# Kernel tuning notes

Measured on AMD Instinct MI355X. Metric: run time of the kernel, lower is better.

Reference implementation:

```python
import jax, jax.numpy as jnp
import numpy as np

B, L, D = 4, 2048, 2048
NH, HD, K = 32, 64, 16
LR = 1.0
EPS = 1e-6


def ln_fwd(x, gamma, beta):
    mu = x.mean(-1, keepdims=True)
    var = jnp.var(x, axis=-1, keepdims=True)
    x_hat = (x - mu) / jnp.sqrt(var + EPS)
    return gamma * x_hat + beta


def ln_fused_l2_bwd(x, target, gamma, beta):
    # grad of 0.5*||LN(x)-target||^2 wrt x (matches LayerNormFunction.backward
    # with grad_output = LN(x) - target)
    d = x.shape[-1]
    mu = x.mean(-1, keepdims=True)
    var = jnp.var(x, axis=-1, keepdims=True)
    std = jnp.sqrt(var + EPS)
    x_hat = (x - mu) / std
    y = gamma * x_hat + beta
    g = (y - target) * gamma
    return (d * g - g.sum(-1, keepdims=True) - x_hat * (g * x_hat).sum(-1, keepdims=True)) / (d * std)


def setup_inputs() -> dict:
    key = jax.random.key(0)
    ks = jax.random.split(key, 12)
    s = 0.02
    return {
        "hidden_states": jax.random.normal(ks[0], (B, L, D), jnp.float32),
        "Wq": jax.random.normal(ks[1], (D, D), jnp.float32) * s,
        "Wk": jax.random.normal(ks[2], (D, D), jnp.float32) * s,
        "Wv": jax.random.normal(ks[3], (D, D), jnp.float32) * s,
        "Wo": jax.random.normal(ks[4], (D, D), jnp.float32) * s,
        "linear_weight": jax.random.normal(ks[5], (NH, 1, D), jnp.float32) * s,
        "linear_bias": jnp.zeros((NH, 1), jnp.float32),
        "ln_weight": jnp.ones((NH, HD), jnp.float32),
        "ln_bias": jnp.zeros((NH, HD), jnp.float32),
        "W1_init": jax.random.normal(ks[6], (NH, HD, HD), jnp.float32) * s,
        "b1_init": jnp.zeros((NH, 1, HD), jnp.float32),
    }


def reference(hidden_states, Wq, Wk, Wv, Wo, linear_weight, linear_bias,
              ln_weight, ln_bias, W1_init, b1_init):
    Bq, Lq, Dq = hidden_states.shape
    n_chunk = Lq // K

    def split(x):  # [B,L,D] -> [B,NH,n_chunk,K,HD]
        return x.reshape(Bq, n_chunk, K, NH, HD).transpose(0, 3, 1, 2, 4)

    XC = split(hidden_states @ Wq.T)
    XB = split(hidden_states @ Wk.T)
    XA = split(hidden_states @ Wv.T)

    # inner-loop learning-rate coefficient: [B,NH,n_chunk,K,1]
    X = hidden_states.reshape(Bq, n_chunk, K, Dq)
    ilr = jnp.einsum('bnkd,hd->bhnk', X, linear_weight[:, 0, :]) + linear_bias[:, 0][None, :, None, None]
    ilr_gated = jax.nn.sigmoid(ilr)[..., None]
    token_idx = 1.0 / jnp.arange(1, K + 1, dtype=hidden_states.dtype)
    coeff = (LR * token_idx).reshape(1, 1, 1, K, 1) * ilr_gated / HD

    ln_w = ln_weight.reshape(1, NH, 1, HD)
    ln_b = ln_bias.reshape(1, NH, 1, HD)
    mask = jnp.tril(jnp.ones((K, K), hidden_states.dtype))

    W1 = jnp.broadcast_to(W1_init[None], (Bq, NH, HD, HD))
    b1 = jnp.broadcast_to(b1_init[None], (Bq, NH, 1, HD))

    def step(carry, inp):
        W1, b1 = carry
        xc, xb, xa, co = inp  # [B,NH,K,HD], co: [B,NH,K,1]
        Z1 = xb @ W1 + b1
        grad = ln_fused_l2_bwd(Z1, xa - xb, ln_w, ln_b)  # [B,NH,K,HD]
        Attn = mask * jnp.einsum('bhkf,bhjf->bhkj', xc, xb)
        E = mask * co.transpose(0, 1, 3, 2)  # E[i,j] = coeff_j * (j<=i)
        b1_bar = b1 - E @ grad
        Z1_bar = xc @ W1 - (Attn * E) @ grad + b1_bar
        W1_new = W1 - jnp.einsum('bhkf,bhkg->bhfg', co * xb, grad)
        b1_new = b1 - (co * grad).sum(-2, keepdims=True)
        out = xc + ln_fwd(Z1_bar, ln_w, ln_b)
        return (W1_new, b1_new), out

    xs = (XC.transpose(2, 0, 1, 3, 4), XB.transpose(2, 0, 1, 3, 4),
          XA.transpose(2, 0, 1, 3, 4), coeff.transpose(2, 0, 1, 3, 4))
    (_, _), outs = jax.lax.scan(step, (W1, b1), xs)
    # outs: [n_chunk,B,NH,K,HD] -> [B,L,D]
    XCW = outs.transpose(1, 0, 3, 2, 4).reshape(Bq, Lq, Dq)
    return XCW @ Wo.T
```

## Files before the change

kernel.cpp:

```cpp
#include <hip/hip_runtime.h>


typedef __attribute__((ext_vector_type(4))) float float4v;
typedef __attribute__((ext_vector_type(8))) __bf16 bf16x8;
typedef __attribute__((ext_vector_type(4))) short short4v;
typedef __attribute__((ext_vector_type(4))) unsigned int uint4v;

__device__ __forceinline__ unsigned short f2bf(float f) {
  unsigned int u = __builtin_bit_cast(unsigned int, f);
  u += 0x7FFFu + ((u >> 16) & 1u);
  return (unsigned short)(u >> 16);
}
__device__ __forceinline__ float bf2f(unsigned short s) {
  unsigned int u = ((unsigned int)s) << 16;
  return __builtin_bit_cast(float, u);
}
__device__ __forceinline__ void lds_load16(const void* g, void* l) {
  __builtin_amdgcn_global_load_lds((const __attribute__((address_space(1))) void*)g,
                                   (__attribute__((address_space(3))) void*)l, 16, 0, 0);
}

__device__ __forceinline__ void store_out(float* p, float v) { *p = v; }
__device__ __forceinline__ void store_out(unsigned short* p, float v) { *p = f2bf(v); }

template <typename OUT>
__global__ __launch_bounds__(256) void gemm_bt(
    const unsigned short* __restrict__ A, const unsigned short* __restrict__ B,
    OUT* __restrict__ C, int M, int N, int K) {
  __shared__ unsigned short sA[128 * 32];
  __shared__ unsigned short sB[128 * 32];
  const int tid = threadIdx.x;
  const int wave = tid >> 6;
  const int lane = tid & 63;
  const int quad = lane >> 4;
  const int l15 = lane & 15;
  const int wm = (wave >> 1) * 64;
  const int wn = (wave & 1) * 64;
  const int bm = blockIdx.y * 128;
  const int bn = blockIdx.x * 128;

  float4v acc[4][4];
#pragma unroll
  for (int i = 0; i < 4; ++i)
#pragma unroll
    for (int j = 0; j < 4; ++j) acc[i][j] = (float4v){0.f, 0.f, 0.f, 0.f};

  const int srow = tid >> 2;
  const int scol = (tid & 3) * 8;
  const unsigned short* aptr = A + (size_t)(bm + srow) * K + scol;
  const unsigned short* bptr = B + (size_t)(bn + srow) * K + scol;
  unsigned short* sAw0 = &sA[wave * 512];
  unsigned short* sAw1 = &sA[2048 + wave * 512];
  unsigned short* sBw0 = &sB[wave * 512];
  unsigned short* sBw1 = &sB[2048 + wave * 512];
  const size_t astep = (size_t)64 * K;

  for (int kt = 0; kt < K; kt += 32) {
    __syncthreads();
    lds_load16(aptr + kt, sAw0);
    lds_load16(aptr + kt + astep, sAw1);
    lds_load16(bptr + kt, sBw0);
    lds_load16(bptr + kt + astep, sBw1);
    __syncthreads();
    bf16x8 af[4], bf[4];
#pragma unroll
    for (int i = 0; i < 4; ++i)
      af[i] = *(const bf16x8*)&sA[(wm + i * 16 + l15) * 32 + quad * 8];
#pragma unroll
    for (int j = 0; j < 4; ++j)
      bf[j] = *(const bf16x8*)&sB[(wn + j * 16 + l15) * 32 + quad * 8];
#pragma unroll
    for (int i = 0; i < 4; ++i)
#pragma unroll
      for (int j = 0; j < 4; ++j)
        acc[i][j] = __builtin_amdgcn_mfma_f32_16x16x32_bf16(af[i], bf[j], acc[i][j], 0, 0, 0);
  }

#pragma unroll
  for (int i = 0; i < 4; ++i) {
    const int row0 = bm + wm + i * 16 + quad * 4;
#pragma unroll
    for (int j = 0; j < 4; ++j) {
      const int col = bn + wn + j * 16 + l15;
#pragma unroll
      for (int r = 0; r < 4; ++r)
        store_out(&C[(size_t)(row0 + r) * N + col], acc[i][j][r]);
    }
  }
}

__global__ __launch_bounds__(256) void f32_to_bf16_k(const float* __restrict__ s,
                                                     unsigned short* __restrict__ d, int n) {
  const int i = (blockIdx.x * 256 + threadIdx.x) * 8;
  if (i >= n) return;
  const float4v a = *(const float4v*)(s + i);
  const float4v b = *(const float4v*)(s + i + 4);
  uint4v o;
  o[0] = (unsigned int)f2bf(a[0]) | ((unsigned int)f2bf(a[1]) << 16);
  o[1] = (unsigned int)f2bf(a[2]) | ((unsigned int)f2bf(a[3]) << 16);
  o[2] = (unsigned int)f2bf(b[0]) | ((unsigned int)f2bf(b[1]) << 16);
  o[3] = (unsigned int)f2bf(b[2]) | ((unsigned int)f2bf(b[3]) << 16);
  *(uint4v*)(d + i) = o;
}

__global__ __launch_bounds__(256) void coeff_k(const unsigned short* __restrict__ ilr,
                                               const float* __restrict__ lb,
                                               float* __restrict__ coeff) {
  const int gid = blockIdx.x * 256 + threadIdx.x;
  const int row = gid >> 5;
  const int h = gid & 31;
  const float v = bf2f(ilr[row * 128 + h]) + lb[h];
  const float sig = 1.0f / (1.0f + __expf(-v));
  const int b = row >> 11;
  const int pos = row & 2047;
  const int cc = pos >> 4;
  const int k = pos & 15;
  coeff[((((size_t)b * 32 + h) * 128 + cc) << 4) + k] = sig / (64.0f * (float)(k + 1));
}

__global__ __launch_bounds__(64, 1) void ttt_scan(
    const unsigned short* __restrict__ XC, const unsigned short* __restrict__ XB,
    const unsigned short* __restrict__ XA, const float* __restrict__ coeff,
    const float* __restrict__ lnw, const float* __restrict__ lnb,
    const float* __restrict__ W1i, const float* __restrict__ b1i,
    unsigned short* __restrict__ XCW) {
  const int b = blockIdx.x >> 5;
  const int h = blockIdx.x & 31;
  const int lane = threadIdx.x;
  const int quad = lane >> 4;
  const int l15 = lane & 15;

  __shared__ float sW1T[64 * 68];
  __shared__ float sXCs[16 * 68];
  __shared__ float sXBs[16 * 68];
  __shared__ float sTs[16 * 68];
  __shared__ float sAttn[16 * 20];
  __shared__ float sB1[64];

  float gam[4], bet[4];
#pragma unroll
  for (int nt = 0; nt < 4; ++nt) {
    gam[nt] = lnw[h * 64 + nt * 16 + l15];
    bet[nt] = lnb[h * 64 + nt * 16 + l15];
  }
  float4v W1r[16];
#pragma unroll
  for (int mt = 0; mt < 4; ++mt)
#pragma unroll
    for (int nt = 0; nt < 4; ++nt) {
      float4v v;
#pragma unroll
      for (int r = 0; r < 4; ++r)
        v[r] = W1i[(size_t)h * 4096 + (size_t)(mt * 16 + quad * 4 + r) * 64 + nt * 16 + l15];
      W1r[mt * 4 + nt] = v;
    }
  sB1[lane] = b1i[h * 64 + lane];

  const int srow = lane >> 2;
  const int scol = (lane & 3) * 16;
  const size_t hdoff = (size_t)h * 64;
  const size_t browoff = (size_t)b * 2048;
  const size_t cobase = (((size_t)b * 32 + h) * 128) * 16;
  const float inv64 = 1.0f / 64.0f;
  const float4v zero4 = {0.f, 0.f, 0.f, 0.f};

  uint4v pxc0, pxc1, pxb0, pxb1, pxa0, pxa1;
  float pco;
  {
    const size_t goff = (browoff + (size_t)srow) * 2048 + hdoff + scol;
    pxc0 = *(const uint4v*)(XC + goff);
    pxc1 = *(const uint4v*)(XC + goff + 8);
    pxb0 = *(const uint4v*)(XB + goff);
    pxb1 = *(const uint4v*)(XB + goff + 8);
    pxa0 = *(const uint4v*)(XA + goff);
    pxa1 = *(const uint4v*)(XA + goff + 8);
    pco = coeff[cobase + l15];
  }

  for (int c = 0; c < 128; ++c) {
    const uint4v xc0 = pxc0, xc1 = pxc1, xb0 = pxb0, xb1 = pxb1, xa0 = pxa0, xa1 = pxa1;
    const float co = pco;
    {
      const int cn = (c < 127) ? c + 1 : 127;
      const size_t goff = (browoff + (size_t)(cn * 16 + srow)) * 2048 + hdoff + scol;
      pxc0 = *(const uint4v*)(XC + goff);
      pxc1 = *(const uint4v*)(XC + goff + 8);
      pxb0 = *(const uint4v*)(XB + goff);
      pxb1 = *(const uint4v*)(XB + goff + 8);
      pxa0 = *(const uint4v*)(XA + goff);
      pxa1 = *(const uint4v*)(XA + goff + 8);
      pco = coeff[cobase + (size_t)cn * 16 + l15];
    }

    float xcv[16], xbv[16], xav[16];
#pragma unroll
    for (int t2 = 0; t2 < 4; ++t2) {
      xcv[t2 * 2] = __builtin_bit_cast(float, xc0[t2] << 16);
      xcv[t2 * 2 + 1] = __builtin_bit_cast(float, xc0[t2] & 0xFFFF0000u);
      xcv[8 + t2 * 2] = __builtin_bit_cast(float, xc1[t2] << 16);
      xcv[8 + t2 * 2 + 1] = __builtin_bit_cast(float, xc1[t2] & 0xFFFF0000u);
      xbv[t2 * 2] = __builtin_bit_cast(float, xb0[t2] << 16);
      xbv[t2 * 2 + 1] = __builtin_bit_cast(float, xb0[t2] & 0xFFFF0000u);
      xbv[8 + t2 * 2] = __builtin_bit_cast(float, xb1[t2] << 16);
      xbv[8 + t2 * 2 + 1] = __builtin_bit_cast(float, xb1[t2] & 0xFFFF0000u);
      xav[t2 * 2] = __builtin_bit_cast(float, xa0[t2] << 16);
      xav[t2 * 2 + 1] = __builtin_bit_cast(float, xa0[t2] & 0xFFFF0000u);
      xav[8 + t2 * 2] = __builtin_bit_cast(float, xa1[t2] << 16);
      xav[8 + t2 * 2 + 1] = __builtin_bit_cast(float, xa1[t2] & 0xFFFF0000u);
    }
    const int sb = srow * 68 + scol;
#pragma unroll
    for (int e = 0; e < 16; ++e) {
      sXCs[sb + e] = xcv[e];
      sXBs[sb + e] = xbv[e];
      sTs[sb + e] = xav[e] - xbv[e];
    }
#pragma unroll
    for (int mt = 0; mt < 4; ++mt)
#pragma unroll
      for (int nt = 0; nt < 4; ++nt)
        *(float4v*)&sW1T[(nt * 16 + l15) * 68 + mt * 16 + quad * 4] = W1r[mt * 4 + nt];

    bf16x8 xbf[2], xcf[2];
#pragma unroll
    for (int hh = 0; hh < 2; ++hh) {
      const float4v pb0 = *(const float4v*)&sXBs[l15 * 68 + hh * 32 + quad * 8];
      const float4v pb1 = *(const float4v*)&sXBs[l15 * 68 + hh * 32 + quad * 8 + 4];
      const float4v pc0 = *(const float4v*)&sXCs[l15 * 68 + hh * 32 + quad * 8];
      const float4v pc1 = *(const float4v*)&sXCs[l15 * 68 + hh * 32 + quad * 8 + 4];
      bf16x8 fb, fc;
#pragma unroll
      for (int r = 0; r < 4; ++r) {
        fb[r] = (__bf16)pb0[r]; fb[4 + r] = (__bf16)pb1[r];
        fc[r] = (__bf16)pc0[r]; fc[4 + r] = (__bf16)pc1[r];
      }
      xbf[hh] = fb; xcf[hh] = fc;
    }
    bf16x8 w1f[4][2];
#pragma unroll
    for (int nt = 0; nt < 4; ++nt)
#pragma unroll
      for (int hh = 0; hh < 2; ++hh) {
        const float4v p0 = *(const float4v*)&sW1T[(nt * 16 + l15) * 68 + hh * 32 + quad * 8];
        const float4v p1 = *(const float4v*)&sW1T[(nt * 16 + l15) * 68 + hh * 32 + quad * 8 + 4];
        bf16x8 f;
#pragma unroll
        for (int r = 0; r < 4; ++r) { f[r] = (__bf16)p0[r]; f[4 + r] = (__bf16)p1[r]; }
        w1f[nt][hh] = f;
      }
    float cof[4];
#pragma unroll
    for (int r = 0; r < 4; ++r) cof[r] = __shfl(co, quad * 4 + r);
    float b1v[4];
#pragma unroll
    for (int nt = 0; nt < 4; ++nt) b1v[nt] = sB1[nt * 16 + l15];

    float4v z[4];
#pragma unroll
    for (int nt = 0; nt < 4; ++nt) {
      float4v t = __builtin_amdgcn_mfma_f32_16x16x32_bf16(xbf[0], w1f[nt][0], zero4, 0, 0, 0);
      t = __builtin_amdgcn_mfma_f32_16x16x32_bf16(xbf[1], w1f[nt][1], t, 0, 0, 0);
#pragma unroll
      for (int r = 0; r < 4; ++r) t[r] += b1v[nt];
      z[nt] = t;
    }

    float s1[4], s2[4];
#pragma unroll
    for (int r = 0; r < 4; ++r) {
      s1[r] = z[0][r] + z[1][r] + z[2][r] + z[3][r];
      s2[r] = z[0][r] * z[0][r] + z[1][r] * z[1][r] + z[2][r] * z[2][r] + z[3][r] * z[3][r];
    }
#pragma unroll
    for (int m = 1; m <= 8; m <<= 1)
#pragma unroll
      for (int r = 0; r < 4; ++r) {
        s1[r] += __shfl_xor(s1[r], m);
        s2[r] += __shfl_xor(s2[r], m);
      }
    float mu[4], rstd[4];
#pragma unroll
    for (int r = 0; r < 4; ++r) {
      mu[r] = s1[r] * inv64;
      const float var = s2[r] * inv64 - mu[r] * mu[r];
      rstd[r] = rsqrtf(var + 1e-6f);
    }
    float xh[4][4], gg[4][4];
#pragma unroll
    for (int nt = 0; nt < 4; ++nt)
#pragma unroll
      for (int r = 0; r < 4; ++r) {
        const float xhat = (z[nt][r] - mu[r]) * rstd[r];
        xh[nt][r] = xhat;
        const float y = gam[nt] * xhat + bet[nt];
        const float tgt = sTs[(quad * 4 + r) * 68 + nt * 16 + l15];
        gg[nt][r] = (y - tgt) * gam[nt];
      }
    float sg[4], sgx[4];
#pragma unroll
    for (int r = 0; r < 4; ++r) {
      sg[r] = gg[0][r] + gg[1][r] + gg[2][r] + gg[3][r];
      sgx[r] = gg[0][r] * xh[0][r] + gg[1][r] * xh[1][r] + gg[2][r] * xh[2][r] + gg[3][r] * xh[3][r];
    }
#pragma unroll
    for (int m = 1; m <= 8; m <<= 1)
#pragma unroll
      for (int r = 0; r < 4; ++r) {
        sg[r] += __shfl_xor(sg[r], m);
        sgx[r] += __shfl_xor(sgx[r], m);
      }
    float grad[4][4];
    short4v gradb[4];
#pragma unroll
    for (int nt = 0; nt < 4; ++nt)
#pragma unroll
      for (int r = 0; r < 4; ++r) {
        grad[nt][r] = (64.0f * gg[nt][r] - sg[r] - xh[nt][r] * sgx[r]) * (rstd[r] * inv64);
        gradb[nt][r] = (short)f2bf(grad[nt][r]);
      }

    float4v at = __builtin_amdgcn_mfma_f32_16x16x32_bf16(xcf[0], xbf[0], zero4, 0, 0, 0);
    at = __builtin_amdgcn_mfma_f32_16x16x32_bf16(xcf[1], xbf[1], at, 0, 0, 0);
#pragma unroll
    for (int r = 0; r < 4; ++r) sAttn[(quad * 4 + r) * 20 + l15] = at[r];
    const float4v av = *(const float4v*)&sAttn[l15 * 20 + quad * 4];
    short4v m1f;
#pragma unroll
    for (int jj = 0; jj < 4; ++jj) {
      const int k = quad * 4 + jj;
      const float e = (k <= l15) ? cof[jj] : 0.0f;
      m1f[jj] = (short)f2bf(-(av[jj] + 1.0f) * e);
    }

#pragma unroll
    for (int nt = 0; nt < 4; ++nt) {
      float4v t = __builtin_amdgcn_mfma_f32_16x16x32_bf16(xcf[0], w1f[nt][0], zero4, 0, 0, 0);
      t = __builtin_amdgcn_mfma_f32_16x16x32_bf16(xcf[1], w1f[nt][1], t, 0, 0, 0);
      t = __builtin_amdgcn_mfma_f32_16x16x16bf16_1k(m1f, gradb[nt], t, 0, 0, 0);
#pragma unroll
      for (int r = 0; r < 4; ++r) t[r] += b1v[nt];
      z[nt] = t;
    }

#pragma unroll
    for (int r = 0; r < 4; ++r) {
      s1[r] = z[0][r] + z[1][r] + z[2][r] + z[3][r];
      s2[r] = z[0][r] * z[0][r] + z[1][r] * z[1][r] + z[2][r] * z[2][r] + z[3][r] * z[3][r];
    }
#pragma unroll
    for (int m = 1; m <= 8; m <<= 1)
#pragma unroll
      for (int r = 0; r < 4; ++r) {
        s1[r] += __shfl_xor(s1[r], m);
        s2[r] += __shfl_xor(s2[r], m);
      }
#pragma unroll
    for (int r = 0; r < 4; ++r) {
      mu[r] = s1[r] * inv64;
      const float var = s2[r] * inv64 - mu[r] * mu[r];
      rstd[r] = rsqrtf(var + 1e-6f);
    }
#pragma unroll
    for (int nt = 0; nt < 4; ++nt)
#pragma unroll
      for (int r = 0; r < 4; ++r) {
        const float xhat = (z[nt][r] - mu[r]) * rstd[r];
        const float y = gam[nt] * xhat + bet[nt];
        const float o = sXCs[(quad * 4 + r) * 68 + nt * 16 + l15] + y;
        XCW[(browoff + (size_t)(c * 16 + quad * 4 + r)) * 2048 + hdoff + nt * 16 + l15] = f2bf(o);
      }

    float pb[4];
#pragma unroll
    for (int nt = 0; nt < 4; ++nt) {
      pb[nt] = cof[0] * grad[nt][0] + cof[1] * grad[nt][1] + cof[2] * grad[nt][2] + cof[3] * grad[nt][3];
      pb[nt] += __shfl_xor(pb[nt], 16);
      pb[nt] += __shfl_xor(pb[nt], 32);
    }
    if (lane < 16) {
#pragma unroll
      for (int nt = 0; nt < 4; ++nt) sB1[nt * 16 + lane] -= pb[nt];
    }

#pragma unroll
    for (int mt = 0; mt < 4; ++mt) {
      short4v caf;
#pragma unroll
      for (int jj = 0; jj < 4; ++jj)
        caf[jj] = (short)f2bf(-cof[jj] * sXBs[(quad * 4 + jj) * 68 + mt * 16 + l15]);
#pragma unroll
      for (int nt = 0; nt < 4; ++nt)
        W1r[mt * 4 + nt] =
            __builtin_amdgcn_mfma_f32_16x16x16bf16_1k(caf, gradb[nt], W1r[mt * 4 + nt], 0, 0, 0);
    }
  }
}

extern "C" void kernel_launch(void* const* d_in, const int* in_sizes, int n_in,
                              void* d_out, int out_size, void* d_ws, size_t ws_size,
                              hipStream_t stream) {
  const float* hs = (const float*)d_in[0];
  const float* Wq = (const float*)d_in[1];
  const float* Wk = (const float*)d_in[2];
  const float* Wv = (const float*)d_in[3];
  const float* Wo = (const float*)d_in[4];
  const float* lw = (const float*)d_in[5];
  const float* lb = (const float*)d_in[6];
  const float* lnw = (const float*)d_in[7];
  const float* lnb = (const float*)d_in[8];
  const float* W1i = (const float*)d_in[9];
  const float* b1i = (const float*)d_in[10];
  float* out = (float*)d_out;
  char* ws = (char*)d_ws;

  unsigned short* hsb = (unsigned short*)(ws);
  unsigned short* wqb = (unsigned short*)(ws + 33554432);
  unsigned short* wkb = (unsigned short*)(ws + 41943040);
  unsigned short* wvb = (unsigned short*)(ws + 50331648);
  unsigned short* wob = (unsigned short*)(ws + 58720256);
  unsigned short* lwb = (unsigned short*)(ws + 67108864);
  unsigned short* XCb = (unsigned short*)(ws + 67633152);
  unsigned short* XBb = (unsigned short*)(ws + 101187584);
  unsigned short* XAb = (unsigned short*)(ws + 134742016);
  unsigned short* ilrb = (unsigned short*)(ws + 168296448);
  float* coeff = (float*)(ws + 170393600);

  f32_to_bf16_k<<<8192, 256, 0, stream>>>(hs, hsb, 16777216);
  f32_to_bf16_k<<<2048, 256, 0, stream>>>(Wq, wqb, 4194304);
  f32_to_bf16_k<<<2048, 256, 0, stream>>>(Wk, wkb, 4194304);
  f32_to_bf16_k<<<2048, 256, 0, stream>>>(Wv, wvb, 4194304);
  f32_to_bf16_k<<<2048, 256, 0, stream>>>(Wo, wob, 4194304);
  hipMemsetAsync(lwb, 0, 524288, stream);
  f32_to_bf16_k<<<32, 256, 0, stream>>>(lw, lwb, 65536);

  dim3 blk(256);
  dim3 gbig(16, 64);
  gemm_bt<unsigned short><<<gbig, blk, 0, stream>>>(hsb, wqb, XCb, 8192, 2048, 2048);
  gemm_bt<unsigned short><<<gbig, blk, 0, stream>>>(hsb, wkb, XBb, 8192, 2048, 2048);
  gemm_bt<unsigned short><<<gbig, blk, 0, stream>>>(hsb, wvb, XAb, 8192, 2048, 2048);
  gemm_bt<unsigned short><<<dim3(1, 64), blk, 0, stream>>>(hsb, lwb, ilrb, 8192, 128, 2048);
  coeff_k<<<1024, 256, 0, stream>>>(ilrb, lb, coeff);
  ttt_scan<<<128, 64, 0, stream>>>(XCb, XBb, XAb, coeff, lnw, lnb, W1i, b1i, hsb);
  gemm_bt<float><<<gbig, blk, 0, stream>>>(hsb, wob, out, 8192, 2048, 2048);
}
```

Measured before the change: 1.059 ms.

## Store scan tiles as bf16 in LDS, use DPP reductions and register b1

The sequential TTT scan kernel now keeps XC/XB/XA and W1 in LDS as bf16 instead of fp32. MFMA operands load directly as bf16x8 without per-element conversion, and W1 is packed with v_cvt_pk_bf16_f32. Row reductions use DPP moves instead of ds_bpermute shuffles. The attention tile is computed transposed so it stays in registers, and b1 is held in registers, removing LDS round trips. This shortens the per-chunk serial critical path, at some cost in rounding the W1 snapshot the same way as before and recomputing the target from bf16 values.

```diff
diff --git a/kernel.cpp b/kernel.cpp
--- a/kernel.cpp
+++ b/kernel.cpp
@@ -5,6 +5,7 @@
 typedef __attribute__((ext_vector_type(8))) __bf16 bf16x8;
 typedef __attribute__((ext_vector_type(4))) short short4v;
 typedef __attribute__((ext_vector_type(4))) unsigned int uint4v;
+typedef __attribute__((ext_vector_type(2))) unsigned int uint2v;
 
 __device__ __forceinline__ unsigned short f2bf(float f) {
   unsigned int u = __builtin_bit_cast(unsigned int, f);
@@ -22,6 +23,24 @@
 
 __device__ __forceinline__ void store_out(float* p, float v) { *p = v; }
 __device__ __forceinline__ void store_out(unsigned short* p, float v) { *p = f2bf(v); }
+
+template <int CTRL>
+__device__ __forceinline__ float dppmov(float x) {
+  return __builtin_bit_cast(
+      float, __builtin_amdgcn_update_dpp(0, __builtin_bit_cast(int, x), CTRL, 0xF, 0xF, true));
+}
+__device__ __forceinline__ float red16(float x) {
+  x += dppmov<0xB1>(x);
+  x += dppmov<0x4E>(x);
+  x += dppmov<0x124>(x);
+  x += dppmov<0x128>(x);
+  return x;
+}
+__device__ __forceinline__ unsigned int cvtpk_bf16(float lo, float hi) {
+  unsigned int r;
+  asm("v_cvt_pk_bf16_f32 %0, %1, %2" : "=v"(r) : "v"(lo), "v"(hi));
+  return r;
+}
 
 template <typename OUT>
 __global__ __launch_bounds__(256) void gemm_bt(
@@ -130,12 +149,11 @@
   const int quad = lane >> 4;
   const int l15 = lane & 15;
 
-  __shared__ float sW1T[64 * 68];
-  __shared__ float sXCs[16 * 68];
-  __shared__ float sXBs[16 * 68];
-  __shared__ float sTs[16 * 68];
-  __shared__ float sAttn[16 * 20];
-  __shared__ float sB1[64];
+  constexpr int LDW = 88;
+  __shared__ unsigned short sW1[64 * LDW];
+  __shared__ unsigned short sXC[16 * LDW];
+  __shared__ unsigned short sXB[16 * LDW];
+  __shared__ unsigned short sXA[16 * LDW];
 
   float gam[4], bet[4];
 #pragma unroll
@@ -154,18 +172,20 @@
         v[r] = W1i[(size_t)h * 4096 + (size_t)(mt * 16 + quad * 4 + r) * 64 + nt * 16 + l15];
       W1r[mt * 4 + nt] = v;
     }
-  sB1[lane] = b1i[h * 64 + lane];
+  float b1v[4];
+#pragma unroll
+  for (int nt = 0; nt < 4; ++nt) b1v[nt] = b1i[h * 64 + nt * 16 + l15];
 
   const int srow = lane >> 2;
   const int scol = (lane & 3) * 16;
   const size_t hdoff = (size_t)h * 64;
   const size_t browoff = (size_t)b * 2048;
-  const size_t cobase = (((size_t)b * 32 + h) * 128) * 16;
+  const float* cobase = coeff + (((size_t)b * 32 + h) * 128) * 16;
   const float inv64 = 1.0f / 64.0f;
   const float4v zero4 = {0.f, 0.f, 0.f, 0.f};
 
   uint4v pxc0, pxc1, pxb0, pxb1, pxa0, pxa1;
-  float pco;
+  float4v pcof;
   {
     const size_t goff = (browoff + (size_t)srow) * 2048 + hdoff + scol;
     pxc0 = *(const uint4v*)(XC + goff);
@@ -174,12 +194,12 @@
     pxb1 = *(const uint4v*)(XB + goff + 8);
     pxa0 = *(const uint4v*)(XA + goff);
     pxa1 = *(const uint4v*)(XA + goff + 8);
-    pco = coeff[cobase + l15];
+    pcof = *(const float4v*)(cobase + quad * 4);
   }
 
   for (int c = 0; c < 128; ++c) {
     const uint4v xc0 = pxc0, xc1 = pxc1, xb0 = pxb0, xb1 = pxb1, xa0 = pxa0, xa1 = pxa1;
-    const float co = pco;
+    const float4v cof = pcof;
     {
       const int cn = (c < 127) ? c + 1 : 127;
       const size_t goff = (browoff + (size_t)(cn * 16 + srow)) * 2048 + hdoff + scol;
@@ -189,71 +209,42 @@
       pxb1 = *(const uint4v*)(XB + goff + 8);
       pxa0 = *(const uint4v*)(XA + goff);
       pxa1 = *(const uint4v*)(XA + goff + 8);
-      pco = coeff[cobase + (size_t)cn * 16 + l15];
-    }
-
-    float xcv[16], xbv[16], xav[16];
-#pragma unroll
-    for (int t2 = 0; t2 < 4; ++t2) {
-      xcv[t2 * 2] = __builtin_bit_cast(float, xc0[t2] << 16);
-      xcv[t2 * 2 + 1] = __builtin_bit_cast(float, xc0[t2] & 0xFFFF0000u);
-      xcv[8 + t2 * 2] = __builtin_bit_cast(float, xc1[t2] << 16);
-      xcv[8 + t2 * 2 + 1] = __builtin_bit_cast(float, xc1[t2] & 0xFFFF0000u);
-      xbv[t2 * 2] = __builtin_bit_cast(float, xb0[t2] << 16);
-      xbv[t2 * 2 + 1] = __builtin_bit_cast(float, xb0[t2] & 0xFFFF0000u);
-      xbv[8 + t2 * 2] = __builtin_bit_cast(float, xb1[t2] << 16);
-      xbv[8 + t2 * 2 + 1] = __builtin_bit_cast(float, xb1[t2] & 0xFFFF0000u);
-      xav[t2 * 2] = __builtin_bit_cast(float, xa0[t2] << 16);
-      xav[t2 * 2 + 1] = __builtin_bit_cast(float, xa0[t2] & 0xFFFF0000u);
-      xav[8 + t2 * 2] = __builtin_bit_cast(float, xa1[t2] << 16);
-      xav[8 + t2 * 2 + 1] = __builtin_bit_cast(float, xa1[t2] & 0xFFFF0000u);
-    }
-    const int sb = srow * 68 + scol;
-#pragma unroll
-    for (int e = 0; e < 16; ++e) {
-      sXCs[sb + e] = xcv[e];
-      sXBs[sb + e] = xbv[e];
-      sTs[sb + e] = xav[e] - xbv[e];
-    }
+      pcof = *(const float4v*)(cobase + (size_t)cn * 16 + quad * 4);
+    }
+
+    *(uint4v*)&sXC[srow * LDW + scol] = xc0;
+    *(uint4v*)&sXC[srow * LDW + scol + 8] = xc1;
+    *(uint4v*)&sXB[srow * LDW + scol] = xb0;
+    *(uint4v*)&sXB[srow * LDW + scol + 8] = xb1;
+    *(uint4v*)&sXA[srow * LDW + scol] = xa0;
+    *(uint4v*)&sXA[srow * LDW + scol + 8] = xa1;
+
 #pragma unroll
     for (int mt = 0; mt < 4; ++mt)
 #pragma unroll
-      for (int nt = 0; nt < 4; ++nt)
-        *(float4v*)&sW1T[(nt * 16 + l15) * 68 + mt * 16 + quad * 4] = W1r[mt * 4 + nt];
+      for (int nt = 0; nt < 4; ++nt) {
+        const float4v w = W1r[mt * 4 + nt];
+        uint2v p;
+        p[0] = cvtpk_bf16(w[0], w[1]);
+        p[1] = cvtpk_bf16(w[2], w[3]);
+        *(uint2v*)&sW1[(nt * 16 + l15) * LDW + mt * 16 + quad * 4] = p;
+      }
 
     bf16x8 xbf[2], xcf[2];
 #pragma unroll
     for (int hh = 0; hh < 2; ++hh) {
-      const float4v pb0 = *(const float4v*)&sXBs[l15 * 68 + hh * 32 + quad * 8];
-      const float4v pb1 = *(const float4v*)&sXBs[l15 * 68 + hh * 32 + quad * 8 + 4];
-      const float4v pc0 = *(const float4v*)&sXCs[l15 * 68 + hh * 32 + quad * 8];
-      const float4v pc1 = *(const float4v*)&sXCs[l15 * 68 + hh * 32 + quad * 8 + 4];
-      bf16x8 fb, fc;
-#pragma unroll
-      for (int r = 0; r < 4; ++r) {
-        fb[r] = (__bf16)pb0[r]; fb[4 + r] = (__bf16)pb1[r];
-        fc[r] = (__bf16)pc0[r]; fc[4 + r] = (__bf16)pc1[r];
-      }
-      xbf[hh] = fb; xcf[hh] = fc;
+      xbf[hh] = *(const bf16x8*)&sXB[l15 * LDW + hh * 32 + quad * 8];
+      xcf[hh] = *(const bf16x8*)&sXC[l15 * LDW + hh * 32 + quad * 8];
     }
     bf16x8 w1f[4][2];
 #pragma unroll
     for (int nt = 0; nt < 4; ++nt)
 #pragma unroll
-      for (int hh = 0; hh < 2; ++hh) {
-        const float4v p0 = *(const float4v*)&sW1T[(nt * 16 + l15) * 68 + hh * 32 + quad * 8];
-        const float4v p1 = *(const float4v*)&sW1T[(nt * 16 + l15) * 68 + hh * 32 + quad * 8 + 4];
-        bf16x8 f;
-#pragma unroll
-        for (int r = 0; r < 4; ++r) { f[r] = (__bf16)p0[r]; f[4 + r] = (__bf16)p1[r]; }
-        w1f[nt][hh] = f;
-      }
-    float cof[4];
-#pragma unroll
-    for (int r = 0; r < 4; ++r) cof[r] = __shfl(co, quad * 4 + r);
-    float b1v[4];
-#pragma unroll
-    for (int nt = 0; nt < 4; ++nt) b1v[nt] = sB1[nt * 16 + l15];
+      for (int hh = 0; hh < 2; ++hh)
+        w1f[nt][hh] = *(const bf16x8*)&sW1[(nt * 16 + l15) * LDW + hh * 32 + quad * 8];
+
+    float4v at = __builtin_amdgcn_mfma_f32_16x16x32_bf16(xbf[0], xcf[0], zero4, 0, 0, 0);
+    at = __builtin_amdgcn_mfma_f32_16x16x32_bf16(xbf[1], xcf[1], at, 0, 0, 0);
 
     float4v z[4];
 #pragma unroll
@@ -268,16 +259,10 @@
     float s1[4], s2[4];
 #pragma unroll
     for (int r = 0; r < 4; ++r) {
-      s1[r] = z[0][r] + z[1][r] + z[2][r] + z[3][r];
-      s2[r] = z[0][r] * z[0][r] + z[1][r] * z[1][r] + z[2][r] * z[2][r] + z[3][r] * z[3][r];
-    }
-#pragma unroll
-    for (int m = 1; m <= 8; m <<= 1)
-#pragma unroll
-      for (int r = 0; r < 4; ++r) {
-        s1[r] += __shfl_xor(s1[r], m);
-        s2[r] += __shfl_xor(s2[r], m);
-      }
+      s1[r] = red16(z[0][r] + z[1][r] + z[2][r] + z[3][r]);
+      s2[r] = red16(z[0][r] * z[0][r] + z[1][r] * z[1][r] + z[2][r] * z[2][r] +
+                    z[3][r] * z[3][r]);
+    }
     float mu[4], rstd[4];
 #pragma unroll
     for (int r = 0; r < 4; ++r) {
@@ -293,22 +278,17 @@
         const float xhat = (z[nt][r] - mu[r]) * rstd[r];
         xh[nt][r] = xhat;
         const float y = gam[nt] * xhat + bet[nt];
-        const float tgt = sTs[(quad * 4 + r) * 68 + nt * 16 + l15];
+        const int toff = (quad * 4 + r) * LDW + nt * 16 + l15;
+        const float tgt = bf2f(sXA[toff]) - bf2f(sXB[toff]);
         gg[nt][r] = (y - tgt) * gam[nt];
       }
     float sg[4], sgx[4];
 #pragma unroll
     for (int r = 0; r < 4; ++r) {
-      sg[r] = gg[0][r] + gg[1][r] + gg[2][r] + gg[3][r];
-      sgx[r] = gg[0][r] * xh[0][r] + gg[1][r] * xh[1][r] + gg[2][r] * xh[2][r] + gg[3][r] * xh[3][r];
-    }
-#pragma unroll
-    for (int m = 1; m <= 8; m <<= 1)
-#pragma unroll
-      for (int r = 0; r < 4; ++r) {
-        sg[r] += __shfl_xor(sg[r], m);
-        sgx[r] += __shfl_xor(sgx[r], m);
-      }
+      sg[r] = red16(gg[0][r] + gg[1][r] + gg[2][r] + gg[3][r]);
+      sgx[r] = red16(gg[0][r] * xh[0][r] + gg[1][r] * xh[1][r] + gg[2][r] * xh[2][r] +
+                     gg[3][r] * xh[3][r]);
+    }
     float grad[4][4];
     short4v gradb[4];
 #pragma unroll
@@ -319,17 +299,12 @@
         gradb[nt][r] = (short)f2bf(grad[nt][r]);
       }
 
-    float4v at = __builtin_amdgcn_mfma_f32_16x16x32_bf16(xcf[0], xbf[0], zero4, 0, 0, 0);
-    at = __builtin_amdgcn_mfma_f32_16x16x32_bf16(xcf[1], xbf[1], at, 0, 0, 0);
-#pragma unroll
-    for (int r = 0; r < 4; ++r) sAttn[(quad * 4 + r) * 20 + l15] = at[r];
-    const float4v av = *(const float4v*)&sAttn[l15 * 20 + quad * 4];
     short4v m1f;
 #pragma unroll
     for (int jj = 0; jj < 4; ++jj) {
       const int k = quad * 4 + jj;
       const float e = (k <= l15) ? cof[jj] : 0.0f;
-      m1f[jj] = (short)f2bf(-(av[jj] + 1.0f) * e);
+      m1f[jj] = (short)f2bf(-(at[jj] + 1.0f) * e);
     }
 
 #pragma unroll
@@ -344,16 +319,10 @@
 
 #pragma unroll
     for (int r = 0; r < 4; ++r) {
-      s1[r] = z[0][r] + z[1][r] + z[2][r] + z[3][r];
-      s2[r] = z[0][r] * z[0][r] + z[1][r] * z[1][r] + z[2][r] * z[2][r] + z[3][r] * z[3][r];
-    }
-#pragma unroll
-    for (int m = 1; m <= 8; m <<= 1)
-#pragma unroll
-      for (int r = 0; r < 4; ++r) {
-        s1[r] += __shfl_xor(s1[r], m);
-        s2[r] += __shfl_xor(s2[r], m);
-      }
+      s1[r] = red16(z[0][r] + z[1][r] + z[2][r] + z[3][r]);
+      s2[r] = red16(z[0][r] * z[0][r] + z[1][r] * z[1][r] + z[2][r] * z[2][r] +
+                    z[3][r] * z[3][r]);
+    }
 #pragma unroll
     for (int r = 0; r < 4; ++r) {
       mu[r] = s1[r] * inv64;
@@ -366,20 +335,17 @@
       for (int r = 0; r < 4; ++r) {
         const float xhat = (z[nt][r] - mu[r]) * rstd[r];
         const float y = gam[nt] * xhat + bet[nt];
-        const float o = sXCs[(quad * 4 + r) * 68 + nt * 16 + l15] + y;
+        const float o = bf2f(sXC[(quad * 4 + r) * LDW + nt * 16 + l15]) + y;
         XCW[(browoff + (size_t)(c * 16 + quad * 4 + r)) * 2048 + hdoff + nt * 16 + l15] = f2bf(o);
       }
 
-    float pb[4];
 #pragma unroll
     for (int nt = 0; nt < 4; ++nt) {
-      pb[nt] = cof[0] * grad[nt][0] + cof[1] * grad[nt][1] + cof[2] * grad[nt][2] + cof[3] * grad[nt][3];
-      pb[nt] += __shfl_xor(pb[nt], 16);
-      pb[nt] += __shfl_xor(pb[nt], 32);
-    }
-    if (lane < 16) {
-#pragma unroll
-      for (int nt = 0; nt < 4; ++nt) sB1[nt * 16 + lane] -= pb[nt];
+      float pb = cof[0] * grad[nt][0] + cof[1] * grad[nt][1] + cof[2] * grad[nt][2] +
+                 cof[3] * grad[nt][3];
+      pb += __shfl_xor(pb, 16);
+      pb += __shfl_xor(pb, 32);
+      b1v[nt] -= pb;
     }
 
 #pragma unroll
@@ -387,7 +353,7 @@
       short4v caf;
 #pragma unroll
       for (int jj = 0; jj < 4; ++jj)
-        caf[jj] = (short)f2bf(-cof[jj] * sXBs[(quad * 4 + jj) * 68 + mt * 16 + l15]);
+        caf[jj] = (short)f2bf(-cof[jj] * bf2f(sXB[(quad * 4 + jj) * LDW + mt * 16 + l15]));
 #pragma unroll
       for (int nt = 0; nt < 4; ++nt)
         W1r[mt * 4 + nt] =
```

After: 1.012 ms. 1.05x faster.
